# Kernel tuning notes

Hardware: AMD Instinct MI355X
Metric: run time of the kernel (lower is better)

## Reference

```python
import jax, jax.numpy as jnp
import numpy as np
from jax import lax

B, S, H, DK = 8192, 12, 8, 64
DM = H * DK  # d_model = 512


def setup_inputs() -> dict:
    key = jax.random.key(0)
    ks = jax.random.split(key, 7)
    query = jax.random.normal(ks[0], (B, S, DM), jnp.float32)
    key_t = jax.random.normal(ks[1], (B, S, DM), jnp.float32)
    value = jax.random.normal(ks[2], (B, S, DM), jnp.float32)
    mask = jnp.ones((B, S, S), jnp.int32)
    # conv1d12: Conv1d(12, 12, 3, 1, 1) -> weight [out_ch=12, in_ch=12, k=3]
    conv_w = jax.random.normal(ks[3], (S, S, 3), jnp.float32) * 0.1
    conv_b = jax.random.normal(ks[4], (S,), jnp.float32) * 0.1
    # final output projection linears[-1]: Linear(512, 512)
    W_out = jax.random.normal(ks[5], (DM, DM), jnp.float32) * (1.0 / np.sqrt(DM))
    b_out = jax.random.normal(ks[6], (DM,), jnp.float32) * 0.01
    return {"query": query, "key": key_t, "value": value, "mask": mask,
            "conv_w": conv_w, "conv_b": conv_b, "W_out": W_out, "b_out": b_out}


def _neighbor_sums(nodes):
    # nodes: [H, B, S, DK]. convo12 pattern == 3-tap sum over head index with zero ends:
    #   s0 = n0+n1; s_i = n_{i-1}+n_i+n_{i+1} (i=1..6); s7 = n6+n7
    p = jnp.pad(nodes, ((1, 1), (0, 0), (0, 0), (0, 0)))
    return p[:-2] + p[1:-1] + p[2:]  # [H, B, S, DK]


def _conv12(x, w, b):
    # x: [N, S, DK] -> conv over length DK with S channels, kernel 3, pad 1
    y = lax.conv_general_dilated(x, w, window_strides=(1,), padding=[(1, 1)],
                                 dimension_numbers=("NCH", "OIH", "NCH"))
    return y + b[None, :, None]


def reference(query, key, value, mask, conv_w, conv_b, W_out, b_out):
    def split_heads(x):
        # torch.split(x, d_k, -1) over 8 heads -> [H, B, S, DK]
        return jnp.moveaxis(x.reshape(B, S, H, DK), 2, 0)

    def conv_all(x):
        s = _neighbor_sums(split_heads(x)).reshape(H * B, S, DK)
        return _conv12(s, conv_w, conv_b).reshape(H, B, S, DK)

    # reunion: stack heads at dim 1 -> [B, H, S, DK]
    q = jnp.moveaxis(conv_all(query), 0, 1)
    k = jnp.moveaxis(conv_all(key), 0, 1)
    v = jnp.moveaxis(conv_all(value), 0, 1)

    scores = jnp.einsum("bhqd,bhkd->bhqk", q, k) / np.sqrt(DK).astype(np.float32)
    # mask.unsqueeze(1): [B,1,S,S]; masked_fill(mask==0, -1e9)
    scores = jnp.where(mask[:, None, :, :] == 0, jnp.float32(-1e9), scores)
    p = jax.nn.softmax(scores, axis=-1)  # dropout = identity (eval mode)
    x = jnp.einsum("bhqk,bhkd->bhqd", p, v)
    x = jnp.moveaxis(x, 1, 2).reshape(B, S, DM)  # transpose(1,2).view
    return x @ W_out.T + b_out
```

## Files before the change

### kernel.cpp

```cpp
#include <hip/hip_runtime.h>
#include <hip/hip_bf16.h>
#include <math.h>

#define NB 8192
#define NS 12
#define NH 8
#define NDK 64
#define NDM 512

typedef __attribute__((ext_vector_type(8))) short bf16x8;
typedef __attribute__((ext_vector_type(4))) float f32x4;

static __device__ __forceinline__ short f2bfb(float x) {
    __hip_bfloat16 h = __float2bfloat16(x);
    return *(short*)&h;
}
static __device__ __forceinline__ float bfb2f(short s) {
    unsigned u = ((unsigned)(unsigned short)s) << 16;
    return __uint_as_float(u);
}

__global__ __launch_bounds__(512) void wcvt_kernel(const float* __restrict__ W,
                                                   __hip_bfloat16* __restrict__ Wb) {
    int i = blockIdx.x * 512 + threadIdx.x;
    Wb[i] = __float2bfloat16(W[i]);
}

__global__ __launch_bounds__(256) void conv3_kernel(
    const float* __restrict__ gq, const float* __restrict__ gk, const float* __restrict__ gv,
    const float* __restrict__ gcw, const float* __restrict__ gcb,
    short* __restrict__ qc, short* __restrict__ kc, short* __restrict__ vc)
{
    __shared__ __align__(16) float wt[3][12][12];
    __shared__ __align__(16) float bconv[12];

    const int tid = threadIdx.x;
    for (int i = tid; i < 444; i += 256) {
        if (i < 432) {
            int t = i / 144, rem = i - t * 144;
            int s2 = rem / 12, s = rem - s2 * 12;
            wt[t][s2][s] = gcw[s * 36 + s2 * 3 + t];
        } else {
            bconv[i - 432] = gcb[i - 432];
        }
    }
    __syncthreads();

    const int t3   = blockIdx.y;
    const int flat = blockIdx.x * 256 + tid;
    const int b    = flat >> 9;
    const int hd   = flat & 511;
    const int h    = hd >> 6;
    const int d    = hd & 63;

    const float* src = (t3 == 0) ? gq : (t3 == 1) ? gk : gv;
    const float* xb  = src + (size_t)b * (NS * NDM);

    const float fm = (h > 0) ? 1.f : 0.f;
    const float fp = (h < 7) ? 1.f : 0.f;
    const float* pa = xb + h * 64 + d;
    const float* pm = xb + (h > 0 ? h - 1 : h) * 64 + d;
    const float* pp = xb + (h < 7 ? h + 1 : h) * 64 + d;

    f32x4 o0 = *(const f32x4*)&bconv[0];
    f32x4 o1 = *(const f32x4*)&bconv[4];
    f32x4 o2 = *(const f32x4*)&bconv[8];

    #pragma unroll 3
    for (int s2 = 0; s2 < 12; ++s2) {
        float a  = pa[s2 * 512];
        float am = pm[s2 * 512] * fm;
        float ap = pp[s2 * 512] * fp;
        float n0 = a + am + ap;
        float nm = __shfl_up(n0, 1);   if (d == 0)  nm = 0.f;
        float np = __shfl_down(n0, 1); if (d == 63) np = 0.f;
        const f32x4* w0 = (const f32x4*)&wt[0][s2][0];
        const f32x4* w1 = (const f32x4*)&wt[1][s2][0];
        const f32x4* w2 = (const f32x4*)&wt[2][s2][0];
        o0 += w0[0] * nm + w1[0] * n0 + w2[0] * np;
        o1 += w0[1] * nm + w1[1] * n0 + w2[1] * np;
        o2 += w0[2] * nm + w1[2] * n0 + w2[2] * np;
    }

    if (t3 < 2) {
        short* dst = ((t3 == 0) ? qc : kc) + ((size_t)b * NH + h) * (NS * NDK);
        #pragma unroll
        for (int s = 0; s < 4; ++s) dst[s * 64 + d]       = f2bfb(o0[s]);
        #pragma unroll
        for (int s = 0; s < 4; ++s) dst[(s + 4) * 64 + d] = f2bfb(o1[s]);
        #pragma unroll
        for (int s = 0; s < 4; ++s) dst[(s + 8) * 64 + d] = f2bfb(o2[s]);
    } else {
        short* dst = vc + (((size_t)b * NH + h) * NDK + d) * NS;
        short4 p0, p1, p2;
        p0.x = f2bfb(o0[0]); p0.y = f2bfb(o0[1]); p0.z = f2bfb(o0[2]); p0.w = f2bfb(o0[3]);
        p1.x = f2bfb(o1[0]); p1.y = f2bfb(o1[1]); p1.z = f2bfb(o1[2]); p1.w = f2bfb(o1[3]);
        p2.x = f2bfb(o2[0]); p2.y = f2bfb(o2[1]); p2.z = f2bfb(o2[2]); p2.w = f2bfb(o2[3]);
        short4* d4 = (short4*)dst;
        d4[0] = p0; d4[1] = p1; d4[2] = p2;
    }
}

__global__ __launch_bounds__(512) void attn2_kernel(
    const short* __restrict__ qc, const short* __restrict__ kc, const short* __restrict__ vc,
    const int* __restrict__ gmask, const __hip_bfloat16* __restrict__ Wb,
    const float* __restrict__ gbo, float* __restrict__ gout)
{
    __shared__ __align__(16) short abuf[48 * 520];
    __shared__ __align__(16) float probs[NH][12][16];

    const int tid = threadIdx.x;
    const int w   = tid >> 6;
    const int ln  = tid & 63;
    const int d   = ln;
    const int rA  = ln & 15, g = ln >> 4;

    const int b0    = blockIdx.x * 4;
    const int bb    = w & 3;
    const int b     = b0 + bb;
    const int hbase = (w >> 2) * 4;

    const int rAr = (rA < 12) ? rA : 0;

    for (int t = 0; t < 4; ++t) {
        const int h = hbase + t;
        const short* qs = qc + ((size_t)b * NH + h) * (NS * NDK);
        const short* ks = kc + ((size_t)b * NH + h) * (NS * NDK);
        bf16x8 aq0 = *(const bf16x8*)(qs + rAr * 64 + g * 8);
        bf16x8 aq1 = *(const bf16x8*)(qs + rAr * 64 + 32 + g * 8);
        bf16x8 bk0 = *(const bf16x8*)(ks + rAr * 64 + g * 8);
        bf16x8 bk1 = *(const bf16x8*)(ks + rAr * 64 + 32 + g * 8);
        f32x4 sc = {0.f, 0.f, 0.f, 0.f};
        sc = __builtin_amdgcn_mfma_f32_16x16x32_bf16(aq0, bk0, sc, 0, 0, 0);
        sc = __builtin_amdgcn_mfma_f32_16x16x32_bf16(aq1, bk1, sc, 0, 0, 0);

        float vv[12];
        {
            const short4* vp = (const short4*)(vc + (((size_t)b * NH + h) * NDK + d) * NS);
            short4 v0 = vp[0], v1 = vp[1], v2 = vp[2];
            vv[0] = bfb2f(v0.x); vv[1] = bfb2f(v0.y); vv[2]  = bfb2f(v0.z); vv[3]  = bfb2f(v0.w);
            vv[4] = bfb2f(v1.x); vv[5] = bfb2f(v1.y); vv[6]  = bfb2f(v1.z); vv[7]  = bfb2f(v1.w);
            vv[8] = bfb2f(v2.x); vv[9] = bfb2f(v2.y); vv[10] = bfb2f(v2.z); vv[11] = bfb2f(v2.w);
        }

        const int kj = rA;
        const int* mrow = gmask + (size_t)b * 144;
        #pragma unroll
        for (int r = 0; r < 4; ++r) {
            int qi = g * 4 + r;
            float s = sc[r] * 0.125f;
            if (kj >= 12) s = -INFINITY;
            else if (qi < 12 && mrow[qi * 12 + kj] == 0) s = -1e9f;
            float m = s;
            #pragma unroll
            for (int off = 1; off < 16; off <<= 1) m = fmaxf(m, __shfl_xor(m, off, 16));
            float e = __expf(s - m);
            float sum = e;
            #pragma unroll
            for (int off = 1; off < 16; off <<= 1) sum += __shfl_xor(sum, off, 16);
            if (qi < 12) probs[w][qi][kj] = e / sum;
        }

        #pragma unroll
        for (int qi = 0; qi < 12; ++qi) {
            const f32x4* pr = (const f32x4*)&probs[w][qi][0];
            f32x4 p0 = pr[0], p1 = pr[1], p2 = pr[2];
            float acc = 0.f;
            #pragma unroll
            for (int j = 0; j < 4; ++j) acc += p0[j] * vv[j] + p1[j] * vv[j + 4] + p2[j] * vv[j + 8];
            abuf[(bb * 12 + qi) * 520 + h * 64 + d] = f2bfb(acc);
        }
    }
    __syncthreads();

    {
        const short* Ws = (const short*)Wb;
        const int n_lane = w * 64 + rA;
        f32x4 acc[3][4] = {};
        #pragma unroll 4
        for (int kk = 0; kk < 16; ++kk) {
            int k0 = kk * 32 + g * 8;
            bf16x8 af0 = *(const bf16x8*)(abuf + (rA)      * 520 + k0);
            bf16x8 af1 = *(const bf16x8*)(abuf + (16 + rA) * 520 + k0);
            bf16x8 af2 = *(const bf16x8*)(abuf + (32 + rA) * 520 + k0);
            #pragma unroll
            for (int i = 0; i < 4; ++i) {
                bf16x8 bfg = *(const bf16x8*)(Ws + (size_t)(n_lane + i * 16) * NDM + k0);
                acc[0][i] = __builtin_amdgcn_mfma_f32_16x16x32_bf16(af0, bfg, acc[0][i], 0, 0, 0);
                acc[1][i] = __builtin_amdgcn_mfma_f32_16x16x32_bf16(af1, bfg, acc[1][i], 0, 0, 0);
                acc[2][i] = __builtin_amdgcn_mfma_f32_16x16x32_bf16(af2, bfg, acc[2][i], 0, 0, 0);
            }
        }
        float bias[4];
        #pragma unroll
        for (int i = 0; i < 4; ++i) bias[i] = gbo[w * 64 + i * 16 + rA];
        #pragma unroll
        for (int m = 0; m < 3; ++m) {
            #pragma unroll
            for (int i = 0; i < 4; ++i) {
                int n = w * 64 + i * 16 + rA;
                #pragma unroll
                for (int r = 0; r < 4; ++r) {
                    int mg  = m * 16 + g * 4 + r;
                    int bi  = mg / 12, qi = mg - bi * 12;
                    gout[(((size_t)(b0 + bi)) * NS + qi) * NDM + n] = acc[m][i][r] + bias[i];
                }
            }
        }
    }
}

__global__ __launch_bounds__(512) void mha_fused4_kernel(
    const float* __restrict__ gq, const float* __restrict__ gk, const float* __restrict__ gv,
    const int* __restrict__ gmask, const float* __restrict__ gcw, const float* __restrict__ gcb,
    const __hip_bfloat16* __restrict__ Wb, const float* __restrict__ gbo,
    float* __restrict__ gout)
{
    __shared__ __align__(16) float xstage[NS][NDM];
    __shared__ __align__(16) short ovbuf[18432];
    __shared__ __align__(16) float probs[NH][16][16];
    __shared__ __align__(16) float wt[3][12][12];
    __shared__ __align__(16) float bconv[12];

    const int b   = blockIdx.x;
    const int tid = threadIdx.x;
    const int wv  = tid >> 6;
    const int ln  = tid & 63;
    const int h = wv, d = ln;

    if (tid < 432) {
        int t = tid / 144, rem = tid - t * 144;
        int s2 = rem / 12, s = rem - s2 * 12;
        wt[t][s2][s] = gcw[s * 36 + s2 * 3 + t];
    } else if (tid < 444) {
        bconv[tid - 432] = gcb[tid - 432];
    }

    const size_t xoff = (size_t)b * (NS * NDM);
    float vv[12];

    for (int t3 = 0; t3 < 3; ++t3) {
        const float* xb = ((t3 == 0) ? gq : (t3 == 1) ? gk : gv) + xoff;
        {
            const float4* s4 = (const float4*)xb;
            float4* dst4 = (float4*)&xstage[0][0];
            #pragma unroll
            for (int i = 0; i < 3; ++i) dst4[tid + i * 512] = s4[tid + i * 512];
        }
        __syncthreads();

        f32x4 o0 = *(const f32x4*)&bconv[0];
        f32x4 o1 = *(const f32x4*)&bconv[4];
        f32x4 o2 = *(const f32x4*)&bconv[8];
        #pragma unroll 4
        for (int s2 = 0; s2 < 12; ++s2) {
            float c  = xstage[s2][h * 64 + d];
            float cm = (h > 0) ? xstage[s2][(h - 1) * 64 + d] : 0.f;
            float cp = (h < 7) ? xstage[s2][(h + 1) * 64 + d] : 0.f;
            float n0 = c + cm + cp;
            float nm = __shfl_up(n0, 1);   if (d == 0)  nm = 0.f;
            float np = __shfl_down(n0, 1); if (d == 63) np = 0.f;
            const f32x4* w0 = (const f32x4*)&wt[0][s2][0];
            const f32x4* w1 = (const f32x4*)&wt[1][s2][0];
            const f32x4* w2 = (const f32x4*)&wt[2][s2][0];
            o0 += w0[0] * nm + w1[0] * n0 + w2[0] * np;
            o1 += w0[1] * nm + w1[1] * n0 + w2[1] * np;
            o2 += w0[2] * nm + w1[2] * n0 + w2[2] * np;
        }
        if (t3 < 2) {
            __hip_bfloat16* st = (__hip_bfloat16*)(ovbuf + (wv * 2 + t3) * 1152);
            #pragma unroll
            for (int s = 0; s < 4; ++s) st[s * 72 + d]       = __float2bfloat16(o0[s]);
            #pragma unroll
            for (int s = 0; s < 4; ++s) st[(s + 4) * 72 + d] = __float2bfloat16(o1[s]);
            #pragma unroll
            for (int s = 0; s < 4; ++s) st[(s + 8) * 72 + d] = __float2bfloat16(o2[s]);
            __syncthreads();
        } else {
            #pragma unroll
            for (int s = 0; s < 4; ++s) { vv[s] = o0[s]; vv[s + 4] = o1[s]; vv[s + 8] = o2[s]; }
        }
    }

    const short* qsp = ovbuf + (wv * 2 + 0) * 1152;
    const short* ksp = ovbuf + (wv * 2 + 1) * 1152;
    const int rA = ln & 15, g = ln >> 4;
    bf16x8 aq0 = *(const bf16x8*)(qsp + rA * 72 + g * 8);
    bf16x8 aq1 = *(const bf16x8*)(qsp + rA * 72 + 32 + g * 8);
    bf16x8 bk0 = *(const bf16x8*)(ksp + rA * 72 + g * 8);
    bf16x8 bk1 = *(const bf16x8*)(ksp + rA * 72 + 32 + g * 8);
    f32x4 sc = {0.f, 0.f, 0.f, 0.f};
    sc = __builtin_amdgcn_mfma_f32_16x16x32_bf16(aq0, bk0, sc, 0, 0, 0);
    sc = __builtin_amdgcn_mfma_f32_16x16x32_bf16(aq1, bk1, sc, 0, 0, 0);

    const int kj = rA;
    const int* mrow = gmask + (size_t)b * 144;
    #pragma unroll
    for (int r = 0; r < 4; ++r) {
        int qi = g * 4 + r;
        float s = sc[r] * 0.125f;
        if (kj >= 12) s = -INFINITY;
        else if (qi < 12 && mrow[qi * 12 + kj] == 0) s = -1e9f;
        float m = s;
        #pragma unroll
        for (int off = 1; off < 16; off <<= 1) m = fmaxf(m, __shfl_xor(m, off, 16));
        float e = __expf(s - m);
        float sum = e;
        #pragma unroll
        for (int off = 1; off < 16; off <<= 1) sum += __shfl_xor(sum, off, 16);
        probs[wv][qi][kj] = e / sum;
    }

    __syncthreads();

    __hip_bfloat16* ab = (__hip_bfloat16*)ovbuf;
    #pragma unroll
    for (int qi = 0; qi < 12; ++qi) {
        const f32x4* pr = (const f32x4*)&probs[wv][qi][0];
        f32x4 p0 = pr[0], p1 = pr[1], p2 = pr[2];
        float acc = 0.f;
        #pragma unroll
        for (int j = 0; j < 4; ++j) acc += p0[j] * vv[j] + p1[j] * vv[j + 4] + p2[j] * vv[j + 8];
        ab[qi * 520 + h * 64 + d] = __float2bfloat16(acc);
    }
    {
        unsigned* az = (unsigned*)(ovbuf + 12 * 520);
        for (int i = tid; i < 1040; i += 512) az[i] = 0u;
    }
    __syncthreads();

    {
        const short* Ws = (const short*)Wb;
        const short* As = ovbuf;
        f32x4 acc[4] = {};
        const int n_lane = wv * 64 + rA;
        #pragma unroll 4
        for (int kk = 0; kk < 16; ++kk) {
            int k0 = kk * 32 + g * 8;
            bf16x8 af = *(const bf16x8*)(As + rA * 520 + k0);
            #pragma unroll
            for (int i = 0; i < 4; ++i) {
                bf16x8 bfg = *(const bf16x8*)(Ws + (size_t)(n_lane + i * 16) * NDM + k0);
                acc[i] = __builtin_amdgcn_mfma_f32_16x16x32_bf16(af, bfg, acc[i], 0, 0, 0);
            }
        }
        float* outb = gout + (size_t)b * (NS * NDM);
        const int m0 = g * 4;
        #pragma unroll
        for (int i = 0; i < 4; ++i) {
            int n = wv * 64 + i * 16 + rA;
            float bias = gbo[n];
            #pragma unroll
            for (int r = 0; r < 4; ++r) {
                int m = m0 + r;
                if (m < 12) outb[m * NDM + n] = acc[i][r] + bias;
            }
        }
    }
}

extern "C" void kernel_launch(void* const* d_in, const int* in_sizes, int n_in,
                              void* d_out, int out_size, void* d_ws, size_t ws_size,
                              hipStream_t stream) {
    const float* q    = (const float*)d_in[0];
    const float* k    = (const float*)d_in[1];
    const float* v    = (const float*)d_in[2];
    const int*   mask = (const int*)d_in[3];
    const float* cw   = (const float*)d_in[4];
    const float* cb   = (const float*)d_in[5];
    const float* W    = (const float*)d_in[6];
    const float* bo   = (const float*)d_in[7];

    const size_t TEN = (size_t)NB * NH * NS * NDK * sizeof(short);
    const size_t REQ = 3 * TEN + (size_t)NDM * NDM * sizeof(short);

    if (ws_size >= REQ) {
        short* vc = (short*)d_ws;
        short* qc = vc + TEN / sizeof(short);
        short* kc = qc + TEN / sizeof(short);
        __hip_bfloat16* Wb = (__hip_bfloat16*)(kc + TEN / sizeof(short));

        hipLaunchKernelGGL(wcvt_kernel, dim3(512), dim3(512), 0, stream, W, Wb);
        hipLaunchKernelGGL(conv3_kernel, dim3(NB * 512 / 256, 3), dim3(256), 0, stream,
                           q, k, v, cw, cb, qc, kc, vc);
        hipLaunchKernelGGL(attn2_kernel, dim3(NB / 4), dim3(512), 0, stream,
                           qc, kc, vc, mask, Wb, bo, (float*)d_out);
    } else {
        __hip_bfloat16* Wb = (__hip_bfloat16*)d_ws;
        hipLaunchKernelGGL(wcvt_kernel, dim3(512), dim3(512), 0, stream, W, Wb);
        hipLaunchKernelGGL(mha_fused4_kernel, dim3(NB), dim3(512), 0, stream,
                           q, k, v, mask, cw, cb, Wb, bo, (float*)d_out);
    }
}
```

Baseline: 531.6 us.

## Fuse conv and attention per batch, write bf16 attention output for projection

The pipeline is restructured. Conv and attention now run in one kernel, one block per batch item, keeping conv outputs in shared memory instead of writing q/k/v to global memory. The P·V product moves from scalar FMAs onto MFMA with bf16 probabilities, and the bf16 attention output is written to a workspace that a separate projection kernel reads. This cuts global traffic from three bf16 intermediates to one. The cost is quantizing the probabilities to bf16 and more shared memory per block.

```diff
diff --git a/kernel.cpp b/kernel.cpp
--- a/kernel.cpp
+++ b/kernel.cpp
@@ -15,10 +15,6 @@
     __hip_bfloat16 h = __float2bfloat16(x);
     return *(short*)&h;
 }
-static __device__ __forceinline__ float bfb2f(short s) {
-    unsigned u = ((unsigned)(unsigned short)s) << 16;
-    return __uint_as_float(u);
-}
 
 __global__ __launch_bounds__(512) void wcvt_kernel(const float* __restrict__ W,
                                                    __hip_bfloat16* __restrict__ Wb) {
@@ -26,149 +22,173 @@
     Wb[i] = __float2bfloat16(W[i]);
 }
 
-__global__ __launch_bounds__(256) void conv3_kernel(
+__global__ __launch_bounds__(512) void fca_kernel(
     const float* __restrict__ gq, const float* __restrict__ gk, const float* __restrict__ gv,
-    const float* __restrict__ gcw, const float* __restrict__ gcb,
-    short* __restrict__ qc, short* __restrict__ kc, short* __restrict__ vc)
+    const int* __restrict__ gmask, const float* __restrict__ gcw, const float* __restrict__ gcb,
+    short* __restrict__ ao)
 {
+    __shared__ __align__(16) short ovl[8 * 2520];
+    __shared__ __align__(16) short pbuf[NH][16][24];
     __shared__ __align__(16) float wt[3][12][12];
     __shared__ __align__(16) float bconv[12];
 
     const int tid = threadIdx.x;
-    for (int i = tid; i < 444; i += 256) {
-        if (i < 432) {
-            int t = i / 144, rem = i - t * 144;
-            int s2 = rem / 12, s = rem - s2 * 12;
-            wt[t][s2][s] = gcw[s * 36 + s2 * 3 + t];
-        } else {
-            bconv[i - 432] = gcb[i - 432];
-        }
-    }
-    __syncthreads();
-
-    const int t3   = blockIdx.y;
-    const int flat = blockIdx.x * 256 + tid;
-    const int b    = flat >> 9;
-    const int hd   = flat & 511;
-    const int h    = hd >> 6;
-    const int d    = hd & 63;
-
-    const float* src = (t3 == 0) ? gq : (t3 == 1) ? gk : gv;
-    const float* xb  = src + (size_t)b * (NS * NDM);
+    const int w   = tid >> 6;
+    const int ln  = tid & 63;
+    const int h = w, d = ln;
+    const int rA  = ln & 15, g = ln >> 4;
+    const int b = blockIdx.x;
+
+    if (tid < 432) {
+        int t = tid / 144, rem = tid - t * 144;
+        int s2 = rem / 12, s = rem - s2 * 12;
+        wt[t][s2][s] = gcw[s * 36 + s2 * 3 + t];
+    } else if (tid < 444) {
+        bconv[tid - 432] = gcb[tid - 432];
+    }
+
+    short* stq  = ovl + w * 2520;
+    short* stk  = stq + 864;
+    short* vbuf = stk + 864;
+
+    if (ln < 24) vbuf[768 + ln] = 0;
+
+    __syncthreads();
 
     const float fm = (h > 0) ? 1.f : 0.f;
     const float fp = (h < 7) ? 1.f : 0.f;
-    const float* pa = xb + h * 64 + d;
-    const float* pm = xb + (h > 0 ? h - 1 : h) * 64 + d;
-    const float* pp = xb + (h < 7 ? h + 1 : h) * 64 + d;
-
-    f32x4 o0 = *(const f32x4*)&bconv[0];
-    f32x4 o1 = *(const f32x4*)&bconv[4];
-    f32x4 o2 = *(const f32x4*)&bconv[8];
-
-    #pragma unroll 3
-    for (int s2 = 0; s2 < 12; ++s2) {
-        float a  = pa[s2 * 512];
-        float am = pm[s2 * 512] * fm;
-        float ap = pp[s2 * 512] * fp;
-        float n0 = a + am + ap;
-        float nm = __shfl_up(n0, 1);   if (d == 0)  nm = 0.f;
-        float np = __shfl_down(n0, 1); if (d == 63) np = 0.f;
-        const f32x4* w0 = (const f32x4*)&wt[0][s2][0];
-        const f32x4* w1 = (const f32x4*)&wt[1][s2][0];
-        const f32x4* w2 = (const f32x4*)&wt[2][s2][0];
-        o0 += w0[0] * nm + w1[0] * n0 + w2[0] * np;
-        o1 += w0[1] * nm + w1[1] * n0 + w2[1] * np;
-        o2 += w0[2] * nm + w1[2] * n0 + w2[2] * np;
-    }
-
-    if (t3 < 2) {
-        short* dst = ((t3 == 0) ? qc : kc) + ((size_t)b * NH + h) * (NS * NDK);
-        #pragma unroll
-        for (int s = 0; s < 4; ++s) dst[s * 64 + d]       = f2bfb(o0[s]);
-        #pragma unroll
-        for (int s = 0; s < 4; ++s) dst[(s + 4) * 64 + d] = f2bfb(o1[s]);
-        #pragma unroll
-        for (int s = 0; s < 4; ++s) dst[(s + 8) * 64 + d] = f2bfb(o2[s]);
-    } else {
-        short* dst = vc + (((size_t)b * NH + h) * NDK + d) * NS;
-        short4 p0, p1, p2;
-        p0.x = f2bfb(o0[0]); p0.y = f2bfb(o0[1]); p0.z = f2bfb(o0[2]); p0.w = f2bfb(o0[3]);
-        p1.x = f2bfb(o1[0]); p1.y = f2bfb(o1[1]); p1.z = f2bfb(o1[2]); p1.w = f2bfb(o1[3]);
-        p2.x = f2bfb(o2[0]); p2.y = f2bfb(o2[1]); p2.z = f2bfb(o2[2]); p2.w = f2bfb(o2[3]);
-        short4* d4 = (short4*)dst;
-        d4[0] = p0; d4[1] = p1; d4[2] = p2;
-    }
-}
-
-__global__ __launch_bounds__(512) void attn2_kernel(
-    const short* __restrict__ qc, const short* __restrict__ kc, const short* __restrict__ vc,
-    const int* __restrict__ gmask, const __hip_bfloat16* __restrict__ Wb,
+    const size_t xoff = (size_t)b * (NS * NDM);
+
+    for (int t3 = 0; t3 < 3; ++t3) {
+        const float* xb = ((t3 == 0) ? gq : (t3 == 1) ? gk : gv) + xoff;
+        const float* pa = xb + h * 64 + d;
+        const float* pm = xb + (h > 0 ? h - 1 : h) * 64 + d;
+        const float* pp = xb + (h < 7 ? h + 1 : h) * 64 + d;
+
+        f32x4 o0 = *(const f32x4*)&bconv[0];
+        f32x4 o1 = *(const f32x4*)&bconv[4];
+        f32x4 o2 = *(const f32x4*)&bconv[8];
+        #pragma unroll 3
+        for (int s2 = 0; s2 < 12; ++s2) {
+            float a  = pa[s2 * 512];
+            float am = pm[s2 * 512] * fm;
+            float ap = pp[s2 * 512] * fp;
+            float n0 = a + am + ap;
+            float nm = __shfl_up(n0, 1);   if (d == 0)  nm = 0.f;
+            float np = __shfl_down(n0, 1); if (d == 63) np = 0.f;
+            const f32x4* w0 = (const f32x4*)&wt[0][s2][0];
+            const f32x4* w1 = (const f32x4*)&wt[1][s2][0];
+            const f32x4* w2 = (const f32x4*)&wt[2][s2][0];
+            o0 += w0[0] * nm + w1[0] * n0 + w2[0] * np;
+            o1 += w0[1] * nm + w1[1] * n0 + w2[1] * np;
+            o2 += w0[2] * nm + w1[2] * n0 + w2[2] * np;
+        }
+        if (t3 < 2) {
+            short* st = (t3 == 0) ? stq : stk;
+            #pragma unroll
+            for (int s = 0; s < 4; ++s) {
+                st[s * 72 + d]       = f2bfb(o0[s]);
+                st[(s + 4) * 72 + d] = f2bfb(o1[s]);
+                st[(s + 8) * 72 + d] = f2bfb(o2[s]);
+            }
+        } else {
+            short4 p0, p1, p2;
+            p0.x = f2bfb(o0[0]); p0.y = f2bfb(o0[1]); p0.z = f2bfb(o0[2]); p0.w = f2bfb(o0[3]);
+            p1.x = f2bfb(o1[0]); p1.y = f2bfb(o1[1]); p1.z = f2bfb(o1[2]); p1.w = f2bfb(o1[3]);
+            p2.x = f2bfb(o2[0]); p2.y = f2bfb(o2[1]); p2.z = f2bfb(o2[2]); p2.w = f2bfb(o2[3]);
+            short4* dst4 = (short4*)(vbuf + d * 12);
+            dst4[0] = p0; dst4[1] = p1; dst4[2] = p2;
+        }
+        __builtin_amdgcn_sched_barrier(0);
+    }
+
+    const int rAr = (rA < 12) ? rA : 0;
+    bf16x8 aq0 = *(const bf16x8*)(stq + rAr * 72 + g * 8);
+    bf16x8 aq1 = *(const bf16x8*)(stq + rAr * 72 + 32 + g * 8);
+    bf16x8 bk0 = *(const bf16x8*)(stk + rAr * 72 + g * 8);
+    bf16x8 bk1 = *(const bf16x8*)(stk + rAr * 72 + 32 + g * 8);
+    f32x4 sc = {0.f, 0.f, 0.f, 0.f};
+    sc = __builtin_amdgcn_mfma_f32_16x16x32_bf16(aq0, bk0, sc, 0, 0, 0);
+    sc = __builtin_amdgcn_mfma_f32_16x16x32_bf16(aq1, bk1, sc, 0, 0, 0);
+
+    const int kj = rA;
+    const int* mrow = gmask + (size_t)b * 144;
+    #pragma unroll
+    for (int r = 0; r < 4; ++r) {
+        int qi = g * 4 + r;
+        float s = sc[r] * 0.125f;
+        if (kj >= 12) s = -INFINITY;
+        else if (qi < 12 && mrow[qi * 12 + kj] == 0) s = -1e9f;
+        float m = s;
+        #pragma unroll
+        for (int off = 1; off < 16; off <<= 1) m = fmaxf(m, __shfl_xor(m, off, 16));
+        float e = __expf(s - m);
+        float sum = e;
+        #pragma unroll
+        for (int off = 1; off < 16; off <<= 1) sum += __shfl_xor(sum, off, 16);
+        pbuf[w][qi][kj] = f2bfb(e / sum);
+    }
+
+    bf16x8 pfrag = (bf16x8){0, 0, 0, 0, 0, 0, 0, 0};
+    if (g < 2) pfrag = *(const bf16x8*)(&pbuf[w][rA][g * 8]);
+
+    f32x4 pv4[4];
+    #pragma unroll
+    for (int i = 0; i < 4; ++i) {
+        bf16x8 bv = (bf16x8){0, 0, 0, 0, 0, 0, 0, 0};
+        if (g < 2) {
+            const short* p = vbuf + (i * 16 + rA) * 12 + g * 8;
+            short4 lo = *(const short4*)(p);
+            short4 hi = *(const short4*)(p + 4);
+            bv[0] = lo.x; bv[1] = lo.y; bv[2] = lo.z; bv[3] = lo.w;
+            bv[4] = hi.x; bv[5] = hi.y; bv[6] = hi.z; bv[7] = hi.w;
+        }
+        f32x4 z = {0.f, 0.f, 0.f, 0.f};
+        pv4[i] = __builtin_amdgcn_mfma_f32_16x16x32_bf16(pfrag, bv, z, 0, 0, 0);
+    }
+
+    __syncthreads();
+
+    short* obuf = ovl;
+    #pragma unroll
+    for (int i = 0; i < 4; ++i) {
+        #pragma unroll
+        for (int r = 0; r < 4; ++r) {
+            int qi = g * 4 + r;
+            if (qi < 12)
+                obuf[qi * 512 + h * 64 + i * 16 + rA] = f2bfb(pv4[i][r]);
+        }
+    }
+    __syncthreads();
+
+    {
+        short* dst = ao + (size_t)b * (NS * NDM);
+        #pragma unroll
+        for (int c = tid; c < 768; c += 512)
+            *(bf16x8*)(dst + c * 8) = *(const bf16x8*)(obuf + c * 8);
+    }
+}
+
+__global__ __launch_bounds__(512) void proj_kernel(
+    const short* __restrict__ ao, const __hip_bfloat16* __restrict__ Wb,
     const float* __restrict__ gbo, float* __restrict__ gout)
 {
     __shared__ __align__(16) short abuf[48 * 520];
-    __shared__ __align__(16) float probs[NH][12][16];
 
     const int tid = threadIdx.x;
     const int w   = tid >> 6;
     const int ln  = tid & 63;
-    const int d   = ln;
     const int rA  = ln & 15, g = ln >> 4;
-
-    const int b0    = blockIdx.x * 4;
-    const int bb    = w & 3;
-    const int b     = b0 + bb;
-    const int hbase = (w >> 2) * 4;
-
-    const int rAr = (rA < 12) ? rA : 0;
-
-    for (int t = 0; t < 4; ++t) {
-        const int h = hbase + t;
-        const short* qs = qc + ((size_t)b * NH + h) * (NS * NDK);
-        const short* ks = kc + ((size_t)b * NH + h) * (NS * NDK);
-        bf16x8 aq0 = *(const bf16x8*)(qs + rAr * 64 + g * 8);
-        bf16x8 aq1 = *(const bf16x8*)(qs + rAr * 64 + 32 + g * 8);
-        bf16x8 bk0 = *(const bf16x8*)(ks + rAr * 64 + g * 8);
-        bf16x8 bk1 = *(const bf16x8*)(ks + rAr * 64 + 32 + g * 8);
-        f32x4 sc = {0.f, 0.f, 0.f, 0.f};
-        sc = __builtin_amdgcn_mfma_f32_16x16x32_bf16(aq0, bk0, sc, 0, 0, 0);
-        sc = __builtin_amdgcn_mfma_f32_16x16x32_bf16(aq1, bk1, sc, 0, 0, 0);
-
-        float vv[12];
-        {
-            const short4* vp = (const short4*)(vc + (((size_t)b * NH + h) * NDK + d) * NS);
-            short4 v0 = vp[0], v1 = vp[1], v2 = vp[2];
-            vv[0] = bfb2f(v0.x); vv[1] = bfb2f(v0.y); vv[2]  = bfb2f(v0.z); vv[3]  = bfb2f(v0.w);
-            vv[4] = bfb2f(v1.x); vv[5] = bfb2f(v1.y); vv[6]  = bfb2f(v1.z); vv[7]  = bfb2f(v1.w);
-            vv[8] = bfb2f(v2.x); vv[9] = bfb2f(v2.y); vv[10] = bfb2f(v2.z); vv[11] = bfb2f(v2.w);
-        }
-
-        const int kj = rA;
-        const int* mrow = gmask + (size_t)b * 144;
-        #pragma unroll
-        for (int r = 0; r < 4; ++r) {
-            int qi = g * 4 + r;
-            float s = sc[r] * 0.125f;
-            if (kj >= 12) s = -INFINITY;
-            else if (qi < 12 && mrow[qi * 12 + kj] == 0) s = -1e9f;
-            float m = s;
-            #pragma unroll
-            for (int off = 1; off < 16; off <<= 1) m = fmaxf(m, __shfl_xor(m, off, 16));
-            float e = __expf(s - m);
-            float sum = e;
-            #pragma unroll
-            for (int off = 1; off < 16; off <<= 1) sum += __shfl_xor(sum, off, 16);
-            if (qi < 12) probs[w][qi][kj] = e / sum;
-        }
-
-        #pragma unroll
-        for (int qi = 0; qi < 12; ++qi) {
-            const f32x4* pr = (const f32x4*)&probs[w][qi][0];
-            f32x4 p0 = pr[0], p1 = pr[1], p2 = pr[2];
-            float acc = 0.f;
-            #pragma unroll
-            for (int j = 0; j < 4; ++j) acc += p0[j] * vv[j] + p1[j] * vv[j + 4] + p2[j] * vv[j + 8];
-            abuf[(bb * 12 + qi) * 520 + h * 64 + d] = f2bfb(acc);
+    const int b0  = blockIdx.x * 4;
+
+    {
+        const short* src = ao + (size_t)b0 * (NS * NDM);
+        #pragma unroll
+        for (int j = 0; j < 6; ++j) {
+            int c   = tid + j * 512;
+            int row = c >> 6;
+            int col = (c & 63) * 8;
+            *(bf16x8*)(abuf + row * 520 + col) = *(const bf16x8*)(src + c * 8);
         }
     }
     __syncthreads();
@@ -371,20 +391,18 @@
     const float* W    = (const float*)d_in[6];
     const float* bo   = (const float*)d_in[7];
 
-    const size_t TEN = (size_t)NB * NH * NS * NDK * sizeof(short);
-    const size_t REQ = 3 * TEN + (size_t)NDM * NDM * sizeof(short);
-
-    if (ws_size >= REQ) {
-        short* vc = (short*)d_ws;
-        short* qc = vc + TEN / sizeof(short);
-        short* kc = qc + TEN / sizeof(short);
-        __hip_bfloat16* Wb = (__hip_bfloat16*)(kc + TEN / sizeof(short));
+    const size_t AOB = (size_t)NB * NS * NDM * sizeof(short);
+    const size_t WBS = (size_t)NDM * NDM * sizeof(short);
+
+    if (ws_size >= AOB + WBS) {
+        short* ao = (short*)d_ws;
+        __hip_bfloat16* Wb = (__hip_bfloat16*)((char*)d_ws + AOB);
 
         hipLaunchKernelGGL(wcvt_kernel, dim3(512), dim3(512), 0, stream, W, Wb);
-        hipLaunchKernelGGL(conv3_kernel, dim3(NB * 512 / 256, 3), dim3(256), 0, stream,
-                           q, k, v, cw, cb, qc, kc, vc);
-        hipLaunchKernelGGL(attn2_kernel, dim3(NB / 4), dim3(512), 0, stream,
-                           qc, kc, vc, mask, Wb, bo, (float*)d_out);
+        hipLaunchKernelGGL(fca_kernel, dim3(NB), dim3(512), 0, stream,
+                           q, k, v, mask, cw, cb, ao);
+        hipLaunchKernelGGL(proj_kernel, dim3(NB / 4), dim3(512), 0, stream,
+                           ao, Wb, bo, (float*)d_out);
     } else {
         __hip_bfloat16* Wb = (__hip_bfloat16*)d_ws;
         hipLaunchKernelGGL(wcvt_kernel, dim3(512), dim3(512), 0, stream, W, Wb);
```

Measured after the change: 597.1 us. +12.3%, slower.
